# Optimization experiments

Hardware: AMD Instinct MI355X
Metric: run time of the kernel (lower is better)

Reference implementation:

```python
import jax, jax.numpy as jnp
import numpy as np

S = 128          # hidden mul for 0e and 1o in the GVP
M_OUT = 256      # 2*n_dets*el_emb_dim = 2*8*16
N_DETS = 8
FACTOR = 2 * N_DETS  # mul_to_axis factor = 16
EPS = 1e-8


def _gvp_layer(s, v, Wh, Wu, Wm, bm, activate):
    # s: (..., S) scalars (0e); v: (..., S, 3) vectors (1o)
    Vh = jnp.einsum('...mt,mh->...ht', v, Wh)                 # hidden vectors
    vn = jnp.sqrt(jnp.sum(Vh * Vh, axis=-1) + EPS)            # invariant norms
    sm = jnp.concatenate([s, vn], axis=-1) @ Wm + bm          # scalar channel
    Vu = jnp.einsum('...ht,ho->...ot', Vh, Wu)
    if activate:
        return jax.nn.silu(sm), Vu * jax.nn.sigmoid(sm)[..., None]
    return sm, Vu  # activate_final=False


def _gvp_mlp(x, params):
    s = x[..., :S]
    v = x[..., S:].reshape(x.shape[:-1] + (S, 3))
    n = len(params)
    for i, (Wh, Wu, Wm, bm) in enumerate(params):
        s, v = _gvp_layer(s, v, Wh, Wu, Wm, bm, activate=(i < n - 1))
    return s, v


def _anti_mlp(x, params):
    # antisymmetrize_e3_func: odd part under parity (1o components negated)
    s1, v1 = _gvp_mlp(x, params)
    xp = jnp.concatenate([x[..., :S], -x[..., S:]], axis=-1)
    s2, v2 = _gvp_mlp(xp, params)
    return 0.5 * (s1 - s2), 0.5 * (v1 - v2)


def setup_inputs() -> dict:
    key = jax.random.key(0)
    ks = jax.random.split(key, 11)
    B, NEL = 2048, 16
    f32 = jnp.float32
    inp = {
        'mo_coeffs': jax.random.normal(ks[0], (B, NEL, S * 4), dtype=f32),
        # GVP layer 0
        'Wh0': jax.random.normal(ks[1], (S, S), f32) / np.sqrt(S),
        'Wu0': jax.random.normal(ks[2], (S, S), f32) / np.sqrt(S),
        'Wm0': jax.random.normal(ks[3], (2 * S, S), f32) / np.sqrt(2 * S),
        'bm0': jnp.zeros((S,), f32),
        # GVP layer 1 (final, no activation)
        'Wh1': jax.random.normal(ks[4], (S, S), f32) / np.sqrt(S),
        'Wu1': jax.random.normal(ks[5], (S, S), f32) / np.sqrt(S),
        'Wm1': jax.random.normal(ks[6], (2 * S, S), f32) / np.sqrt(2 * S),
        'bm1': jnp.zeros((S,), f32),
        # NamedE3Linear: one weight per irrep block (0e and 1o)
        'W0': jax.random.normal(ks[7], (S, M_OUT), f32),
        'W1': jax.random.normal(ks[8], (S, M_OUT), f32),
    }
    return inp


def reference(mo_coeffs, Wh0, Wu0, Wm0, bm0, Wh1, Wu1, Wm1, bm1, W0, W1):
    params = [(Wh0, Wu0, Wm0, bm0), (Wh1, Wu1, Wm1, bm1)]
    s, v = _anti_mlp(mo_coeffs, params)           # (...,128), (...,128,3)
    inv_sqrt = 1.0 / np.sqrt(S).astype(np.float32)
    so = (s @ W0) * inv_sqrt                      # (..., 256)   0e block
    vo = jnp.einsum('...mt,mn->...nt', v, W1) * inv_sqrt  # (...,256,3) 1o block
    lead = so.shape[:-1]
    # mul_to_axis(16): mul 256 -> (16, 16); per-irrep flat dims concatenated
    so = so.reshape(lead + (FACTOR, M_OUT // FACTOR))            # (...,16,16)
    vo = vo.reshape(lead + (FACTOR, (M_OUT // FACTOR) * 3))      # (...,16,48)
    bf = jnp.concatenate([so, vo], axis=-1)                      # (...,16,64)
    # final reshape: (..., 2*n_dets, d) -> (..., 2, n_dets, d)
    bf = bf.reshape(lead + (2, N_DETS, bf.shape[-1]))
    return bf
```

## Files before the change

### kernel.cpp

```cpp
#include <hip/hip_runtime.h>
#include <hip/hip_bf16.h>


typedef __attribute__((ext_vector_type(8))) short short8;
typedef __attribute__((ext_vector_type(4))) float floatx4;

static __device__ __forceinline__ unsigned short f2bf(float f) {
  unsigned u = __float_as_uint(f);
  u = (u + 0x7fffu + ((u >> 16) & 1u)) >> 16;
  return (unsigned short)u;
}
static __device__ __forceinline__ unsigned pk2(float lo, float hi) {
  __hip_bfloat162 h = __float22bfloat162_rn(make_float2(lo, hi));
  return *(unsigned*)&h;
}

static __device__ __forceinline__ void put_sw(unsigned short* B, int k, int n,
                                              float val, int KT) {
  int kt = k >> 5, quad = (k >> 3) & 3, j = k & 7;
  int nt = n >> 4, c = n & 15;
  int lane = quad * 16 + c;
  B[(((nt * KT + kt) * 64 + lane) << 3) + j] = f2bf(val);
}

__global__ __launch_bounds__(128) void prep1(
    const float* __restrict__ Wh0, const float* __restrict__ Wu0,
    const float* __restrict__ Wh1, const float* __restrict__ Wu1,
    unsigned short* __restrict__ Wcat_sw, float* __restrict__ T) {
  int b = blockIdx.x, o = threadIdx.x;
  if (b < 128) {
    int m = b;
    float acc = 0.f;
    for (int h = 0; h < 128; ++h) acc += Wh0[m * 128 + h] * Wu0[h * 128 + o];
    put_sw(Wcat_sw, m, o, Wh0[m * 128 + o], 4);
    put_sw(Wcat_sw, m, o + 128, acc, 4);
  } else {
    int m = b - 128;
    float acc = 0.f;
    for (int h = 0; h < 128; ++h) acc += Wh1[m * 128 + h] * Wu1[h * 128 + o];
    T[m * 128 + o] = acc;
  }
}

__global__ __launch_bounds__(256) void prep2(
    const float* __restrict__ T, const float* __restrict__ W1,
    const float* __restrict__ Wm0, unsigned short* __restrict__ C_sw,
    unsigned short* __restrict__ Wm0_sw) {
  int b = blockIdx.x, tid = threadIdx.x;
  if (b < 128) {
    int m = b, n = tid;
    float acc = 0.f;
    for (int h = 0; h < 128; ++h) acc += T[m * 128 + h] * W1[h * 256 + n];
    put_sw(C_sw, m, n, acc * 0.08838834764831845f, 4);
  } else {
    int k = (b - 128) * 2 + (tid >> 7);
    int n = tid & 127;
    put_sw(Wm0_sw, k, n, Wm0[k * 128 + n], 8);
  }
}

#define XA_S 264
#define XV_S 136
#define XV_T 2176

__global__ __launch_bounds__(256, 4) void main_k(
    const float* __restrict__ x, const float* __restrict__ bm0,
    const unsigned short* __restrict__ Wcat_sw,
    const unsigned short* __restrict__ Wm0_sw,
    const unsigned short* __restrict__ C_sw, float* __restrict__ out) {
  __shared__ __align__(16) unsigned char smem[34560];
  unsigned short* v1 = (unsigned short*)smem;
  unsigned short* xa = (unsigned short*)(smem + 13056);
  unsigned short* xv = (unsigned short*)(smem + 21504);

  const int tid = threadIdx.x;
  const int lane = tid & 63;
  const int w = tid >> 6;
  const int l15 = lane & 15;
  const int quad = lane >> 4;
  const int r0 = blockIdx.x << 4;
  const float* xrow = x + (size_t)r0 * 512;
  const int ntg[4] = {2 * w, 2 * w + 1, 8 + 2 * w, 9 + 2 * w};

  float bias0 = bm0[(2 * w) * 16 + l15];
  float bias1 = bm0[(2 * w + 1) * 16 + l15];

#pragma unroll
  for (int i = 0; i < 2; ++i) {
    int e = tid + 256 * i;
    int r = e >> 5, c0 = (e & 31) << 2;
    float4 s4 = *(const float4*)(xrow + r * 512 + c0);
    uint2 p = make_uint2(pk2(s4.x, s4.y), pk2(s4.z, s4.w));
    *(uint2*)(xa + r * XA_S + c0) = p;
  }
#pragma unroll
  for (int i = 0; i < 2; ++i) {
    int e = tid + 256 * i;
    int r = e >> 5, mc = e & 31;
    const float* p = xrow + r * 512 + 128 + mc * 12;
    float4 a = *(const float4*)(p);
    float4 b = *(const float4*)(p + 4);
    float4 c = *(const float4*)(p + 8);
    float f[12] = {a.x, a.y, a.z, a.w, b.x, b.y, b.z, b.w, c.x, c.y, c.z, c.w};
#pragma unroll
    for (int t = 0; t < 3; ++t) {
      uint2 pk = make_uint2(pk2(f[t], f[t + 3]), pk2(f[t + 6], f[t + 9]));
      *(uint2*)(xv + t * XV_T + r * XV_S + mc * 4) = pk;
    }
  }
  __syncthreads();

  const floatx4 zf4 = {0.f, 0.f, 0.f, 0.f};

  floatx4 acc[3][4];
#pragma unroll
  for (int t = 0; t < 3; ++t)
#pragma unroll
    for (int j = 0; j < 4; ++j) acc[t][j] = zf4;
  for (int kt = 0; kt < 4; ++kt) {
    short8 bf[4];
#pragma unroll
    for (int j = 0; j < 4; ++j)
      bf[j] = *(const short8*)(Wcat_sw + (((ntg[j] * 4 + kt) * 64 + lane) << 3));
#pragma unroll
    for (int t = 0; t < 3; ++t) {
      short8 af = *(const short8*)(xv + t * XV_T + l15 * XV_S + kt * 32 + quad * 8);
#pragma unroll
      for (int j = 0; j < 4; ++j)
        acc[t][j] = __builtin_amdgcn_mfma_f32_16x16x32_bf16(af, bf[j], acc[t][j], 0, 0, 0);
    }
  }

#pragma unroll
  for (int j = 0; j < 2; ++j)
#pragma unroll
    for (int rg = 0; rg < 4; ++rg) {
      float s0 = acc[0][j][rg], s1 = acc[1][j][rg], s2 = acc[2][j][rg];
      float vn = sqrtf(s0 * s0 + s1 * s1 + s2 * s2 + 1e-8f);
      int r = quad * 4 + rg;
      int h = ntg[j] * 16 + l15;
      xa[r * XA_S + 128 + h] = f2bf(vn);
    }
  __syncthreads();

  floatx4 ga[2] = {zf4, zf4};
  for (int kt = 0; kt < 8; ++kt) {
    short8 af = *(const short8*)(xa + l15 * XA_S + kt * 32 + quad * 8);
    short8 b0 = *(const short8*)(Wm0_sw + ((((2 * w) * 8 + kt) * 64 + lane) << 3));
    short8 b1 = *(const short8*)(Wm0_sw + ((((2 * w + 1) * 8 + kt) * 64 + lane) << 3));
    ga[0] = __builtin_amdgcn_mfma_f32_16x16x32_bf16(af, b0, ga[0], 0, 0, 0);
    ga[1] = __builtin_amdgcn_mfma_f32_16x16x32_bf16(af, b1, ga[1], 0, 0, 0);
  }
  float g[2][4];
#pragma unroll
  for (int j = 0; j < 2; ++j) {
    float bias = j ? bias1 : bias0;
#pragma unroll
    for (int rg = 0; rg < 4; ++rg)
      g[j][rg] = 1.f / (1.f + __expf(-(ga[j][rg] + bias)));
  }
#pragma unroll
  for (int t = 0; t < 3; ++t)
#pragma unroll
    for (int j = 0; j < 2; ++j)
#pragma unroll
      for (int rg = 0; rg < 4; ++rg) {
        int r = quad * 4 + rg;
        int o = (2 * w + j) * 16 + l15;
        v1[t * XV_T + r * XV_S + o] = f2bf(acc[t][2 + j][rg] * g[j][rg]);
      }
  __syncthreads();

  floatx4 vacc[3][4];
#pragma unroll
  for (int t = 0; t < 3; ++t)
#pragma unroll
    for (int j = 0; j < 4; ++j) vacc[t][j] = zf4;
  for (int kt = 0; kt < 4; ++kt) {
    short8 bf[4];
#pragma unroll
    for (int j = 0; j < 4; ++j)
      bf[j] = *(const short8*)(C_sw + (((ntg[j] * 4 + kt) * 64 + lane) << 3));
#pragma unroll
    for (int t = 0; t < 3; ++t) {
      short8 af = *(const short8*)(v1 + t * XV_T + l15 * XV_S + kt * 32 + quad * 8);
#pragma unroll
      for (int j = 0; j < 4; ++j)
        vacc[t][j] = __builtin_amdgcn_mfma_f32_16x16x32_bf16(af, bf[j], vacc[t][j], 0, 0, 0);
    }
  }

  float* orow = out + (size_t)r0 * 1024;
#pragma unroll
  for (int i = 0; i < 4; ++i) {
    int e = tid + 256 * i;
    int r = e >> 6, gblk = (e >> 2) & 15, s4 = e & 3;
    *(float4*)(orow + (size_t)r * 1024 + gblk * 64 + s4 * 4) =
        make_float4(0.f, 0.f, 0.f, 0.f);
  }
#pragma unroll
  for (int j = 0; j < 4; ++j) {
    int nt = ntg[j];
#pragma unroll
    for (int rg = 0; rg < 4; ++rg) {
      int r = quad * 4 + rg;
      *(float3*)(orow + (size_t)r * 1024 + nt * 64 + 16 + 3 * l15) =
          make_float3(vacc[0][j][rg], vacc[1][j][rg], vacc[2][j][rg]);
    }
  }
}

extern "C" void kernel_launch(void* const* d_in, const int* in_sizes, int n_in,
                              void* d_out, int out_size, void* d_ws,
                              size_t ws_size, hipStream_t stream) {
  const float* mo = (const float*)d_in[0];
  const float* Wh0 = (const float*)d_in[1];
  const float* Wu0 = (const float*)d_in[2];
  const float* Wm0 = (const float*)d_in[3];
  const float* bm0 = (const float*)d_in[4];
  const float* Wh1 = (const float*)d_in[5];
  const float* Wu1 = (const float*)d_in[6];
  const float* W1 = (const float*)d_in[10];

  unsigned short* ws = (unsigned short*)d_ws;
  unsigned short* Wcat_sw = ws;
  unsigned short* C_sw = ws + 32768;
  unsigned short* Wm0_sw = ws + 65536;
  float* T = (float*)(ws + 98304);

  prep1<<<256, 128, 0, stream>>>(Wh0, Wu0, Wh1, Wu1, Wcat_sw, T);
  prep2<<<256, 256, 0, stream>>>(T, W1, Wm0, C_sw, Wm0_sw);

  main_k<<<2048, 256, 0, stream>>>(mo, bm0, Wcat_sw, Wm0_sw, C_sw,
                                   (float*)d_out);
}
```

Measured before the change: 225.5 us.

## Alias xv with v1 in LDS and split MFMA accumulators to raise occupancy

```diff
diff --git a/kernel.cpp b/kernel.cpp
--- a/kernel.cpp
+++ b/kernel.cpp
@@ -63,15 +63,15 @@
 #define XV_S 136
 #define XV_T 2176
 
-__global__ __launch_bounds__(256, 4) void main_k(
+__global__ __launch_bounds__(256, 5) void main_k(
     const float* __restrict__ x, const float* __restrict__ bm0,
     const unsigned short* __restrict__ Wcat_sw,
     const unsigned short* __restrict__ Wm0_sw,
     const unsigned short* __restrict__ C_sw, float* __restrict__ out) {
-  __shared__ __align__(16) unsigned char smem[34560];
+  __shared__ __align__(16) unsigned char smem[21504];
+  unsigned short* xv = (unsigned short*)smem;
   unsigned short* v1 = (unsigned short*)smem;
   unsigned short* xa = (unsigned short*)(smem + 13056);
-  unsigned short* xv = (unsigned short*)(smem + 21504);
 
   const int tid = threadIdx.x;
   const int lane = tid & 63;
@@ -80,6 +80,7 @@
   const int quad = lane >> 4;
   const int r0 = blockIdx.x << 4;
   const float* xrow = x + (size_t)r0 * 512;
+  float* orow = out + (size_t)r0 * 1024;
   const int ntg[4] = {2 * w, 2 * w + 1, 8 + 2 * w, 9 + 2 * w};
 
   float bias0 = bm0[(2 * w) * 16 + l15];
@@ -111,23 +112,29 @@
   __syncthreads();
 
   const floatx4 zf4 = {0.f, 0.f, 0.f, 0.f};
-
-  floatx4 acc[3][4];
+#pragma unroll
+  for (int i = 0; i < 4; ++i) {
+    int e = tid + 256 * i;
+    int r = e >> 6, gblk = (e >> 2) & 15, s4i = e & 3;
+    *(floatx4*)(orow + (size_t)r * 1024 + gblk * 64 + s4i * 4) = zf4;
+  }
+
+  floatx4 accH[3][2];
 #pragma unroll
   for (int t = 0; t < 3; ++t)
 #pragma unroll
-    for (int j = 0; j < 4; ++j) acc[t][j] = zf4;
+    for (int j = 0; j < 2; ++j) accH[t][j] = zf4;
   for (int kt = 0; kt < 4; ++kt) {
-    short8 bf[4];
-#pragma unroll
-    for (int j = 0; j < 4; ++j)
+    short8 bf[2];
+#pragma unroll
+    for (int j = 0; j < 2; ++j)
       bf[j] = *(const short8*)(Wcat_sw + (((ntg[j] * 4 + kt) * 64 + lane) << 3));
 #pragma unroll
     for (int t = 0; t < 3; ++t) {
       short8 af = *(const short8*)(xv + t * XV_T + l15 * XV_S + kt * 32 + quad * 8);
 #pragma unroll
-      for (int j = 0; j < 4; ++j)
-        acc[t][j] = __builtin_amdgcn_mfma_f32_16x16x32_bf16(af, bf[j], acc[t][j], 0, 0, 0);
+      for (int j = 0; j < 2; ++j)
+        accH[t][j] = __builtin_amdgcn_mfma_f32_16x16x32_bf16(af, bf[j], accH[t][j], 0, 0, 0);
     }
   }
 
@@ -135,12 +142,31 @@
   for (int j = 0; j < 2; ++j)
 #pragma unroll
     for (int rg = 0; rg < 4; ++rg) {
-      float s0 = acc[0][j][rg], s1 = acc[1][j][rg], s2 = acc[2][j][rg];
+      float s0 = accH[0][j][rg], s1 = accH[1][j][rg], s2 = accH[2][j][rg];
       float vn = sqrtf(s0 * s0 + s1 * s1 + s2 * s2 + 1e-8f);
       int r = quad * 4 + rg;
       int h = ntg[j] * 16 + l15;
       xa[r * XA_S + 128 + h] = f2bf(vn);
     }
+
+  floatx4 accU[3][2];
+#pragma unroll
+  for (int t = 0; t < 3; ++t)
+#pragma unroll
+    for (int j = 0; j < 2; ++j) accU[t][j] = zf4;
+  for (int kt = 0; kt < 4; ++kt) {
+    short8 bf[2];
+#pragma unroll
+    for (int j = 0; j < 2; ++j)
+      bf[j] = *(const short8*)(Wcat_sw + (((ntg[2 + j] * 4 + kt) * 64 + lane) << 3));
+#pragma unroll
+    for (int t = 0; t < 3; ++t) {
+      short8 af = *(const short8*)(xv + t * XV_T + l15 * XV_S + kt * 32 + quad * 8);
+#pragma unroll
+      for (int j = 0; j < 2; ++j)
+        accU[t][j] = __builtin_amdgcn_mfma_f32_16x16x32_bf16(af, bf[j], accU[t][j], 0, 0, 0);
+    }
+  }
   __syncthreads();
 
   floatx4 ga[2] = {zf4, zf4};
@@ -167,45 +193,40 @@
       for (int rg = 0; rg < 4; ++rg) {
         int r = quad * 4 + rg;
         int o = (2 * w + j) * 16 + l15;
-        v1[t * XV_T + r * XV_S + o] = f2bf(acc[t][2 + j][rg] * g[j][rg]);
+        v1[t * XV_T + r * XV_S + o] = f2bf(accU[t][j][rg] * g[j][rg]);
       }
   __syncthreads();
 
-  floatx4 vacc[3][4];
-#pragma unroll
-  for (int t = 0; t < 3; ++t)
-#pragma unroll
-    for (int j = 0; j < 4; ++j) vacc[t][j] = zf4;
-  for (int kt = 0; kt < 4; ++kt) {
-    short8 bf[4];
-#pragma unroll
-    for (int j = 0; j < 4; ++j)
-      bf[j] = *(const short8*)(C_sw + (((ntg[j] * 4 + kt) * 64 + lane) << 3));
-#pragma unroll
-    for (int t = 0; t < 3; ++t) {
-      short8 af = *(const short8*)(v1 + t * XV_T + l15 * XV_S + kt * 32 + quad * 8);
-#pragma unroll
-      for (int j = 0; j < 4; ++j)
-        vacc[t][j] = __builtin_amdgcn_mfma_f32_16x16x32_bf16(af, bf[j], vacc[t][j], 0, 0, 0);
-    }
-  }
-
-  float* orow = out + (size_t)r0 * 1024;
-#pragma unroll
-  for (int i = 0; i < 4; ++i) {
-    int e = tid + 256 * i;
-    int r = e >> 6, gblk = (e >> 2) & 15, s4 = e & 3;
-    *(float4*)(orow + (size_t)r * 1024 + gblk * 64 + s4 * 4) =
-        make_float4(0.f, 0.f, 0.f, 0.f);
-  }
-#pragma unroll
-  for (int j = 0; j < 4; ++j) {
-    int nt = ntg[j];
-#pragma unroll
-    for (int rg = 0; rg < 4; ++rg) {
-      int r = quad * 4 + rg;
-      *(float3*)(orow + (size_t)r * 1024 + nt * 64 + 16 + 3 * l15) =
-          make_float3(vacc[0][j][rg], vacc[1][j][rg], vacc[2][j][rg]);
+#pragma unroll
+  for (int half = 0; half < 2; ++half) {
+    floatx4 vacc[3][2];
+#pragma unroll
+    for (int t = 0; t < 3; ++t)
+#pragma unroll
+      for (int j = 0; j < 2; ++j) vacc[t][j] = zf4;
+    for (int kt = 0; kt < 4; ++kt) {
+      short8 bf[2];
+#pragma unroll
+      for (int j = 0; j < 2; ++j)
+        bf[j] = *(const short8*)(C_sw +
+                                 (((ntg[2 * half + j] * 4 + kt) * 64 + lane) << 3));
+#pragma unroll
+      for (int t = 0; t < 3; ++t) {
+        short8 af = *(const short8*)(v1 + t * XV_T + l15 * XV_S + kt * 32 + quad * 8);
+#pragma unroll
+        for (int j = 0; j < 2; ++j)
+          vacc[t][j] = __builtin_amdgcn_mfma_f32_16x16x32_bf16(af, bf[j], vacc[t][j], 0, 0, 0);
+      }
+    }
+#pragma unroll
+    for (int j = 0; j < 2; ++j) {
+      int nt = ntg[2 * half + j];
+#pragma unroll
+      for (int rg = 0; rg < 4; ++rg) {
+        int r = quad * 4 + rg;
+        *(float3*)(orow + (size_t)r * 1024 + nt * 64 + 16 + 3 * l15) =
+            make_float3(vacc[0][j][rg], vacc[1][j][rg], vacc[2][j][rg]);
+      }
     }
   }
 }
```

Measured after the change: 235.5 us. 4.4% more time.
